# Optimization experiments

Measured on AMD Instinct MI355X. Metric: run time of the kernel, lower is better.

## Reference

```python
import jax, jax.numpy as jnp
import numpy as np

B, S, D, H = 4, 2048, 1024, 16
HS = D // H  # head size = 64


def setup_inputs() -> dict:
    key = jax.random.key(0)
    k1, k2, k3 = jax.random.split(key, 3)
    return {
        "input_data": jax.random.normal(k1, (B, S, D), dtype=jnp.float32),
        "w_qkv": jax.random.normal(k2, (D, 3 * D), dtype=jnp.float32) * (1.0 / np.sqrt(D)),
        "b_qkv": jnp.zeros((3 * D,), dtype=jnp.float32),
        "w_proj": jax.random.normal(k3, (D, D), dtype=jnp.float32) * (1.0 / np.sqrt(D)),
        "b_proj": jnp.zeros((D,), dtype=jnp.float32),
    }


def reference(input_data, w_qkv, b_qkv, w_proj, b_proj):
    b, s, d = input_data.shape
    qkv = input_data @ w_qkv + b_qkv  # [b, s, 3d]
    q, k, v = jnp.split(qkv, 3, axis=-1)
    # [b, h, s, hs]
    q = q.reshape(b, s, H, HS).transpose(0, 2, 1, 3)
    k = k.reshape(b, s, H, HS).transpose(0, 2, 1, 3)
    v = v.reshape(b, s, H, HS).transpose(0, 2, 1, 3)
    # NB: original module scales by 1/sqrt(num_heads), not 1/sqrt(head_size)
    scores = jnp.einsum('bhqd,bhkd->bhqk', q, k) / jnp.sqrt(jnp.float32(H))
    causal = jnp.tril(jnp.ones((s, s), dtype=bool))
    scores = jnp.where(causal[None, None], scores, -jnp.inf)
    weights = jax.nn.softmax(scores, axis=-1)  # dropout p=0.0 -> identity
    out = jnp.einsum('bhqk,bhkd->bhqd', weights, v)
    out = out.transpose(0, 2, 1, 3).reshape(b, s, d)
    return out @ w_proj + b_proj
```

## Files before the change

kernel.cpp:

```cpp
#include <hip/hip_runtime.h>


typedef unsigned short u16;
typedef short bf16x8 __attribute__((ext_vector_type(8)));
typedef unsigned short u16x8 __attribute__((ext_vector_type(8)));
typedef float f32x4 __attribute__((ext_vector_type(4)));
typedef float f32x16 __attribute__((ext_vector_type(16)));

#define S_LEN 2048
#define DMODEL 1024
#define NHEAD 16
#define MROWS 8192

#define SCALE_LOG2E 0.36067376022224085f

#define WAITVM_(N) asm volatile("s_waitcnt vmcnt(" #N ")" ::: "memory")
#define WAITVM(N) WAITVM_(N)

__device__ __forceinline__ u16 f2bf(float f) {
  union { float f; unsigned u; } c; c.f = f;
  unsigned u = c.u;
  u += 0x7fffu + ((u >> 16) & 1u);
  return (u16)(u >> 16);
}

__device__ __forceinline__ float exp2_fast(float x) {
  float r; asm("v_exp_f32 %0, %1" : "=v"(r) : "v"(x)); return r;
}

__device__ __forceinline__ unsigned cvtpk_bf16(float a, float b) {
  unsigned r;
  asm("v_cvt_pk_bf16_f32 %0, %1, %2" : "=v"(r) : "v"(a), "v"(b));
  return r;
}

__device__ __forceinline__ void plswap(unsigned& a, unsigned& b) {
  asm("v_permlane32_swap_b32 %0, %1" : "+v"(a), "+v"(b));
}

__device__ __forceinline__ f32x4 mfma16(bf16x8 a, bf16x8 b, f32x4 c) {
  return __builtin_amdgcn_mfma_f32_16x16x32_bf16(a, b, c, 0, 0, 0);
}

__device__ __forceinline__ f32x16 mfma32(bf16x8 a, bf16x8 b, f32x16 c) {
  return __builtin_amdgcn_mfma_f32_32x32x16_bf16(a, b, c, 0, 0, 0);
}

__device__ __forceinline__ void gload_lds16(const void* g, void* l) {
  __builtin_amdgcn_global_load_lds((__attribute__((address_space(1))) void*)g,
                                   (__attribute__((address_space(3))) void*)l,
                                   16, 0, 0);
}

__global__ void k_f32_to_bf16(const float* __restrict__ in, u16* __restrict__ out, int n) {
  int i = (blockIdx.x * 256 + threadIdx.x) * 4;
  if (i < n) {
    float4 v = *reinterpret_cast<const float4*>(in + i);
    ushort4 o;
    o.x = f2bf(v.x); o.y = f2bf(v.y); o.z = f2bf(v.z); o.w = f2bf(v.w);
    *reinterpret_cast<ushort4*>(out + i) = o;
  }
}

__global__ void k_transpose_to_bf16(const float* __restrict__ in, u16* __restrict__ out,
                                    int K, int N) {
  __shared__ float t[32][33];
  int n0 = blockIdx.x * 32, k0 = blockIdx.y * 32;
  int tx = threadIdx.x & 31, ty = threadIdx.x >> 5;
#pragma unroll
  for (int i = 0; i < 32; i += 8)
    t[ty + i][tx] = in[(size_t)(k0 + ty + i) * N + n0 + tx];
  __syncthreads();
#pragma unroll
  for (int i = 0; i < 32; i += 8)
    out[(size_t)(n0 + ty + i) * K + k0 + tx] = f2bf(t[tx][ty + i]);
}

template <int MODE>
__global__ __launch_bounds__(512, 1) void k_gemm8(const u16* __restrict__ A,
                                                  const u16* __restrict__ Bt,
                                                  const float* __restrict__ bias,
                                                  u16* __restrict__ outb,
                                                  float* __restrict__ outf,
                                                  u16* __restrict__ vtout,
                                                  int N, int K) {
  __shared__ u16 As[3][2][256 * 32];
  __shared__ u16 Bs[3][2][128 * 32];

  const int tid = threadIdx.x;
  const int lane = tid & 63, wave = tid >> 6;
  const int wr = wave >> 1, wc = wave & 1;
  const int lr = lane & 15, lk = lane >> 4;
  const int m0 = blockIdx.x * 256, n0 = blockIdx.y * 128;
  const size_t Kb = (size_t)K * 2;

  const int csw = ((tid & 3) ^ ((tid >> 3) & 3)) * 16;
  const char* Asrc0 = (const char*)A + (size_t)(m0 + (tid >> 2)) * Kb + csw;
  const char* Asrc1 = Asrc0 + 128 * Kb;
  const char* Bsrc0 = (const char*)Bt + (size_t)(n0 + (tid >> 2)) * Kb + csw;

#define STAGE_KH(BUFX, KH, T)                                                  \
  {                                                                            \
    const size_t ko_ = (size_t)(T) * 128 + (KH) * 64;                          \
    gload_lds16(Asrc0 + ko_, &As[BUFX][KH][(size_t)tid * 8]);                  \
    gload_lds16(Asrc1 + ko_, &As[BUFX][KH][((size_t)tid + 512) * 8]);          \
    gload_lds16(Bsrc0 + ko_, &Bs[BUFX][KH][(size_t)tid * 8]);                  \
  }

  f32x4 zero4 = {0.f, 0.f, 0.f, 0.f};
  f32x4 acc[4][4];
#pragma unroll
  for (int m = 0; m < 4; ++m)
#pragma unroll
    for (int n = 0; n < 4; ++n) acc[m][n] = zero4;

  const int slotsw = (lr >> 1) & 3;

#define PHASE(BUFX, KH, VM, DOSTAGE, SBUF, ST)                                 \
  {                                                                            \
    WAITVM(VM);                                                                \
    __builtin_amdgcn_s_barrier();                                              \
    __builtin_amdgcn_sched_barrier(0);                                         \
    bf16x8 af[4], bfr[4];                                                      \
    _Pragma("unroll") for (int m = 0; m < 4; ++m)                              \
        af[m] = *reinterpret_cast<const bf16x8*>(                              \
            &As[BUFX][KH][(wr * 64 + m * 16 + lr) * 32 + ((lk ^ slotsw) * 8)]);\
    _Pragma("unroll") for (int n = 0; n < 4; ++n)                              \
        bfr[n] = *reinterpret_cast<const bf16x8*>(                             \
            &Bs[BUFX][KH][(wc * 64 + n * 16 + lr) * 32 + ((lk ^ slotsw) * 8)]);\
    if (DOSTAGE) STAGE_KH(SBUF, KH, ST);                                       \
    __builtin_amdgcn_sched_barrier(0);                                         \
    __builtin_amdgcn_s_setprio(1);                                             \
    _Pragma("unroll") for (int m = 0; m < 4; ++m)                              \
        _Pragma("unroll") for (int n = 0; n < 4; ++n)                          \
            acc[m][n] = mfma16(af[m], bfr[n], acc[m][n]);                      \
    __builtin_amdgcn_s_setprio(0);                                             \
  }

  const int nkt = K >> 6;
  STAGE_KH(0, 0, 0);
  STAGE_KH(0, 1, 0);
  STAGE_KH(1, 0, 1);
  STAGE_KH(1, 1, 1);

  for (int t = 0; t < nkt - 2; ++t) {
    const int bf3 = t % 3;
    const int bn3 = (t + 2) % 3;
    PHASE(bf3, 0, 6, 1, bn3, t + 2);
    PHASE(bf3, 1, 9, 1, bn3, t + 2);
  }
  {
    const int bf3 = (nkt - 2) % 3;
    PHASE(bf3, 0, 6, 0, 0, 0);
    PHASE(bf3, 1, 6, 0, 0, 0);
  }
  {
    const int bf3 = (nkt - 1) % 3;
    PHASE(bf3, 0, 0, 0, 0, 0);
    PHASE(bf3, 1, 0, 0, 0, 0);
  }
#undef PHASE
#undef STAGE_KH

#pragma unroll
  for (int n = 0; n < 4; ++n) {
    int col = n0 + wc * 64 + n * 16 + lr;
    float bv = bias[col];
#pragma unroll
    for (int m = 0; m < 4; ++m) {
      int rowb = m0 + wr * 64 + m * 16 + lk * 4;
      if (MODE == 1) {
#pragma unroll
        for (int r = 0; r < 4; ++r)
          outf[(size_t)(rowb + r) * N + col] = acc[m][n][r] + bv;
      } else {
        if (col < 2048) {
          const float qs = (col < 1024) ? SCALE_LOG2E : 1.0f;
#pragma unroll
          for (int r = 0; r < 4; ++r)
            outb[(size_t)(rowb + r) * 2048 + col] = f2bf((acc[m][n][r] + bv) * qs);
        } else {
          int hh = (col >> 6) & 15, dd = col & 63;
          int bb = rowb >> 11, ss = rowb & 2047;
          ushort4 o;
          o.x = f2bf(acc[m][n][0] + bv);
          o.y = f2bf(acc[m][n][1] + bv);
          o.z = f2bf(acc[m][n][2] + bv);
          o.w = f2bf(acc[m][n][3] + bv);
          *reinterpret_cast<ushort4*>(
              vtout + ((size_t)(bb * 16 + hh) * 64 + dd) * 2048 + ss) = o;
        }
      }
    }
  }
}

__global__ __launch_bounds__(512, 4) void k_attn11(const u16* __restrict__ qk,
                                                   const u16* __restrict__ vt,
                                                   u16* __restrict__ ao) {
  __shared__ u16 Ks[2][4096];
  __shared__ u16 Vs[2][4096];

  const int tid = threadIdx.x;
  const int lane = tid & 63, wave = tid >> 6;
  const int l31 = lane & 31, hi = lane >> 5;
  const int gid = blockIdx.x;
  const int bh = gid & 63;
  const int tq = gid >> 6;
  const int t = (tq < 4) ? tq : 11 - tq;
  const int b = bh >> 4, h = bh & 15;

  const int q0 = t * 256 + wave * 32;
  const int ktd = (q0 + 31) >> 6;
  const int KTMAX = 4 * t + 3;
  const int qrel = q0 + l31 - ktd * 64;

  bf16x8 qf[4];
  {
    const u16* qp = qk + ((size_t)b * S_LEN + q0 + l31) * 2048 + h * 64 + hi * 8;
#pragma unroll
    for (int ks = 0; ks < 4; ++ks)
      qf[ks] = *reinterpret_cast<const bf16x8*>(qp + ks * 16);
  }

  const int swzcol = 16 * ((lane & 7) ^ (lane >> 3));
  const char* kg = (const char*)qk + ((size_t)b * S_LEN) * 4096 + 2048 + h * 128 +
                   (size_t)(wave * 8 + (lane >> 3)) * 4096 + swzcol;
  const char* vg = (const char*)vt +
                   ((size_t)bh * 64 + wave * 8 + (lane >> 3)) * 4096 + swzcol;

#define STAGE(BUF, KT)                                                   \
  {                                                                      \
    gload_lds16(kg + (size_t)(KT) * 64 * 4096, &Ks[BUF][wave * 512]);    \
    gload_lds16(vg + (size_t)(KT) * 128, &Vs[BUF][wave * 512]);          \
  }

  f32x16 oT[2];
#pragma unroll
  for (int kb = 0; kb < 2; ++kb)
#pragma unroll
    for (int e = 0; e < 16; ++e) oT[kb][e] = 0.f;
  float l_i = 0.f;

  const int rsw = (l31 & 7) << 4;

  STAGE(0, 0);
  int buf = 0;

  for (int kt = 0; kt <= KTMAX; ++kt) {
    if (kt < KTMAX) {
      STAGE(buf ^ 1, kt + 1);
      WAITVM(2);
    } else {
      WAITVM(0);
    }
    __builtin_amdgcn_s_barrier();
    __builtin_amdgcn_sched_barrier(0);

    if (kt <= ktd) {
      const char* Kb = (const char*)&Ks[buf][0];
      const char* Vb = (const char*)&Vs[buf][0];
      const bool masked = (kt == ktd);

      bf16x8 kf[2][4];
#pragma unroll
      for (int kb = 0; kb < 2; ++kb)
#pragma unroll
        for (int ks = 0; ks < 4; ++ks)
          kf[kb][ks] = *reinterpret_cast<const bf16x8*>(
              Kb + (kb * 32 + l31) * 128 + ((ks * 32 + hi * 16) ^ rsw));

      f32x16 sc[2];
      __builtin_amdgcn_s_setprio(1);
#pragma unroll
      for (int kb = 0; kb < 2; ++kb) {
        sc[kb] = mfma32(kf[kb][0], qf[0], f32x16{});
#pragma unroll
        for (int ks = 1; ks < 4; ++ks) sc[kb] = mfma32(kf[kb][ks], qf[ks], sc[kb]);
      }
      __builtin_amdgcn_s_setprio(0);

      bf16x8 vf[2][4];
#pragma unroll
      for (int kbd = 0; kbd < 2; ++kbd)
#pragma unroll
        for (int tt = 0; tt < 4; ++tt)
          vf[kbd][tt] = *reinterpret_cast<const bf16x8*>(
              Vb + (kbd * 32 + l31) * 128 + ((tt * 32 + hi * 16) ^ rsw));

      if (masked) {
#pragma unroll
        for (int kb = 0; kb < 2; ++kb)
#pragma unroll
          for (int e = 0; e < 16; ++e) {
            int key_ = kb * 32 + (e & 3) + ((e >> 2) << 3) + hi * 4;
            if (key_ > qrel) sc[kb][e] = -INFINITY;
          }
      }
      float rsa = 0.f, rsb = 0.f, rsc = 0.f, rsd = 0.f;
      unsigned pk_[8][2];
#pragma unroll
      for (int kb = 0; kb < 2; ++kb)
#pragma unroll
        for (int s = 0; s < 4; ++s) {
          float p0 = exp2_fast(sc[kb][s * 4 + 0]);
          float p1 = exp2_fast(sc[kb][s * 4 + 1]);
          float p2 = exp2_fast(sc[kb][s * 4 + 2]);
          float p3 = exp2_fast(sc[kb][s * 4 + 3]);
          rsa += p0; rsb += p1; rsc += p2; rsd += p3;
          pk_[kb * 4 + s][0] = cvtpk_bf16(p0, p1);
          pk_[kb * 4 + s][1] = cvtpk_bf16(p2, p3);
        }
      l_i += (rsa + rsb) + (rsc + rsd);

      bf16x8 pfr[4];
#pragma unroll
      for (int tt = 0; tt < 4; ++tt) {
        unsigned a0 = pk_[2 * tt][0], b0 = pk_[2 * tt + 1][0];
        unsigned a1 = pk_[2 * tt][1], b1 = pk_[2 * tt + 1][1];
        plswap(a0, b0);
        plswap(a1, b1);
        unsigned fr[4] = {a0, a1, b0, b1};
        pfr[tt] = *reinterpret_cast<const bf16x8*>(&fr[0]);
      }

      __builtin_amdgcn_s_setprio(1);
#pragma unroll
      for (int tt = 0; tt < 4; ++tt) {
        oT[0] = mfma32(vf[0][tt], pfr[tt], oT[0]);
        oT[1] = mfma32(vf[1][tt], pfr[tt], oT[1]);
      }
      __builtin_amdgcn_s_setprio(0);
    }

    __builtin_amdgcn_sched_barrier(0);
    __builtin_amdgcn_s_barrier();
    buf ^= 1;
  }
#undef STAGE

  {
    float lt = l_i + __shfl_xor(l_i, 32, 64);
    float inv = 1.f / lt;
    u16* orow = ao + ((size_t)b * S_LEN + q0 + l31) * DMODEL + h * 64 + hi * 4;
#pragma unroll
    for (int kbd = 0; kbd < 2; ++kbd)
#pragma unroll
      for (int s = 0; s < 4; ++s) {
        unsigned w0 = cvtpk_bf16(oT[kbd][s * 4 + 0] * inv, oT[kbd][s * 4 + 1] * inv);
        unsigned w1 = cvtpk_bf16(oT[kbd][s * 4 + 2] * inv, oT[kbd][s * 4 + 3] * inv);
        *reinterpret_cast<unsigned*>(orow + kbd * 32 + s * 8) = w0;
        *reinterpret_cast<unsigned*>(orow + kbd * 32 + s * 8 + 2) = w1;
      }
  }
}

extern "C" void kernel_launch(void* const* d_in, const int* in_sizes, int n_in,
                              void* d_out, int out_size, void* d_ws, size_t ws_size,
                              hipStream_t stream) {
  const float* x = (const float*)d_in[0];
  const float* wqkv = (const float*)d_in[1];
  const float* bqkv = (const float*)d_in[2];
  const float* wproj = (const float*)d_in[3];
  const float* bproj = (const float*)d_in[4];
  float* out = (float*)d_out;

  char* ws = (char*)d_ws;
  u16* Xb     = (u16*)(ws);
  u16* Wqkvt  = (u16*)(ws + (size_t)16777216);
  u16* Wprojt = (u16*)(ws + (size_t)23068672);
  u16* QKb    = (u16*)(ws + (size_t)25165824);
  u16* Vt     = (u16*)(ws + (size_t)58720256);
  u16* AOb    = (u16*)(ws + (size_t)75497472);

  k_f32_to_bf16<<<MROWS * DMODEL / 4 / 256, 256, 0, stream>>>(x, Xb, MROWS * DMODEL);
  k_transpose_to_bf16<<<dim3(3072 / 32, 1024 / 32), 256, 0, stream>>>(wqkv, Wqkvt, 1024, 3072);
  k_transpose_to_bf16<<<dim3(1024 / 32, 1024 / 32), 256, 0, stream>>>(wproj, Wprojt, 1024, 1024);

  k_gemm8<2><<<dim3(MROWS / 256, 3072 / 128), 512, 0, stream>>>(
      Xb, Wqkvt, bqkv, QKb, nullptr, Vt, 3072, 1024);

  k_attn11<<<dim3(512), 512, 0, stream>>>(QKb, Vt, AOb);

  k_gemm8<1><<<dim3(MROWS / 256, DMODEL / 128), 512, 0, stream>>>(
      AOb, Wprojt, bproj, nullptr, out, nullptr, DMODEL, 1024);
}
```

Baseline: 194.7 us.

## Restructure causal attention into small blocks pairing complementary query tiles

```diff
diff --git a/kernel.cpp b/kernel.cpp
--- a/kernel.cpp
+++ b/kernel.cpp
@@ -195,9 +195,9 @@
   }
 }
 
-__global__ __launch_bounds__(512, 4) void k_attn11(const u16* __restrict__ qk,
-                                                   const u16* __restrict__ vt,
-                                                   u16* __restrict__ ao) {
+__global__ __launch_bounds__(128) void k_attn12(const u16* __restrict__ qk,
+                                                const u16* __restrict__ vt,
+                                                u16* __restrict__ ao) {
   __shared__ u16 Ks[2][4096];
   __shared__ u16 Vs[2][4096];
 
@@ -205,90 +205,109 @@
   const int lane = tid & 63, wave = tid >> 6;
   const int l31 = lane & 31, hi = lane >> 5;
   const int gid = blockIdx.x;
-  const int bh = gid & 63;
-  const int tq = gid >> 6;
-  const int t = (tq < 4) ? tq : 11 - tq;
+  const int bh = gid >> 4, j = gid & 15;
   const int b = bh >> 4, h = bh & 15;
 
-  const int q0 = t * 256 + wave * 32;
-  const int ktd = (q0 + 31) >> 6;
-  const int KTMAX = 4 * t + 3;
-  const int qrel = q0 + l31 - ktd * 64;
-
-  bf16x8 qf[4];
+  const int A = 2 * j + wave;
+  const int Bg = 63 - A;
+  const int ktmax = 31 - j;
+  const int ktdA = j;
+  const int qrelA = ((A & 1) << 5) + l31;
+  const int qrelB = ((Bg & 1) << 5) + l31;
+  const int rowA = 32 * A, rowB = 32 * Bg;
+
+  bf16x8 qfA[4], qfB[4];
   {
-    const u16* qp = qk + ((size_t)b * S_LEN + q0 + l31) * 2048 + h * 64 + hi * 8;
-#pragma unroll
-    for (int ks = 0; ks < 4; ++ks)
-      qf[ks] = *reinterpret_cast<const bf16x8*>(qp + ks * 16);
+    const u16* qa = qk + ((size_t)b * S_LEN + rowA + l31) * 2048 + h * 64 + hi * 8;
+    const u16* qb = qk + ((size_t)b * S_LEN + rowB + l31) * 2048 + h * 64 + hi * 8;
+#pragma unroll
+    for (int ks = 0; ks < 4; ++ks) {
+      qfA[ks] = *reinterpret_cast<const bf16x8*>(qa + ks * 16);
+      qfB[ks] = *reinterpret_cast<const bf16x8*>(qb + ks * 16);
+    }
   }
 
   const int swzcol = 16 * ((lane & 7) ^ (lane >> 3));
   const char* kg = (const char*)qk + ((size_t)b * S_LEN) * 4096 + 2048 + h * 128 +
-                   (size_t)(wave * 8 + (lane >> 3)) * 4096 + swzcol;
+                   (size_t)(wave * 32 + (lane >> 3)) * 4096 + swzcol;
   const char* vg = (const char*)vt +
-                   ((size_t)bh * 64 + wave * 8 + (lane >> 3)) * 4096 + swzcol;
-
-#define STAGE(BUF, KT)                                                   \
-  {                                                                      \
-    gload_lds16(kg + (size_t)(KT) * 64 * 4096, &Ks[BUF][wave * 512]);    \
-    gload_lds16(vg + (size_t)(KT) * 128, &Vs[BUF][wave * 512]);          \
-  }
-
-  f32x16 oT[2];
-#pragma unroll
-  for (int kb = 0; kb < 2; ++kb)
-#pragma unroll
-    for (int e = 0; e < 16; ++e) oT[kb][e] = 0.f;
-  float l_i = 0.f;
+                   ((size_t)bh * 64 + wave * 32 + (lane >> 3)) * 4096 + swzcol;
+
+#define STAGE(BUF, KT)                                                        \
+  {                                                                           \
+    const char* kg_ = kg + (size_t)(KT) * 64 * 4096;                          \
+    const char* vg_ = vg + (size_t)(KT) * 128;                                \
+    _Pragma("unroll") for (int i = 0; i < 4; ++i)                             \
+        gload_lds16(kg_ + (size_t)(8 * i) * 4096,                             \
+                    &Ks[BUF][(wave * 32 + 8 * i) * 64]);                      \
+    _Pragma("unroll") for (int i = 0; i < 4; ++i)                             \
+        gload_lds16(vg_ + (size_t)(8 * i) * 4096,                             \
+                    &Vs[BUF][(wave * 32 + 8 * i) * 64]);                      \
+  }
+
+  f32x16 oT[2][2];
+#pragma unroll
+  for (int g = 0; g < 2; ++g)
+#pragma unroll
+    for (int kb = 0; kb < 2; ++kb)
+#pragma unroll
+      for (int e = 0; e < 16; ++e) oT[g][kb][e] = 0.f;
+  float l_i[2] = {0.f, 0.f};
 
   const int rsw = (l31 & 7) << 4;
 
   STAGE(0, 0);
   int buf = 0;
 
-  for (int kt = 0; kt <= KTMAX; ++kt) {
-    if (kt < KTMAX) {
+  for (int kt = 0; kt <= ktmax; ++kt) {
+    if (kt < ktmax) {
       STAGE(buf ^ 1, kt + 1);
-      WAITVM(2);
+      WAITVM(8);
     } else {
       WAITVM(0);
     }
     __builtin_amdgcn_s_barrier();
     __builtin_amdgcn_sched_barrier(0);
 
-    if (kt <= ktd) {
-      const char* Kb = (const char*)&Ks[buf][0];
-      const char* Vb = (const char*)&Vs[buf][0];
-      const bool masked = (kt == ktd);
-
-      bf16x8 kf[2][4];
-#pragma unroll
-      for (int kb = 0; kb < 2; ++kb)
-#pragma unroll
-        for (int ks = 0; ks < 4; ++ks)
-          kf[kb][ks] = *reinterpret_cast<const bf16x8*>(
-              Kb + (kb * 32 + l31) * 128 + ((ks * 32 + hi * 16) ^ rsw));
+    const char* Kb = (const char*)&Ks[buf][0];
+    const char* Vb = (const char*)&Vs[buf][0];
+
+    bf16x8 kf[2][4];
+#pragma unroll
+    for (int kb = 0; kb < 2; ++kb)
+#pragma unroll
+      for (int ks = 0; ks < 4; ++ks)
+        kf[kb][ks] = *reinterpret_cast<const bf16x8*>(
+            Kb + (kb * 32 + l31) * 128 + ((ks * 32 + hi * 16) ^ rsw));
+
+    bf16x8 vf[2][4];
+#pragma unroll
+    for (int kbd = 0; kbd < 2; ++kbd)
+#pragma unroll
+      for (int tt = 0; tt < 4; ++tt)
+        vf[kbd][tt] = *reinterpret_cast<const bf16x8*>(
+            Vb + (kbd * 32 + l31) * 128 + ((tt * 32 + hi * 16) ^ rsw));
+
+    const bool actA = (kt <= ktdA);
+
+#pragma unroll
+    for (int g = 0; g < 2; ++g) {
+      if (g == 1 && !actA) continue;
+      const bool msk = (g == 0) ? (kt == ktmax) : (kt == ktdA);
+      const int qrel = (g == 0) ? qrelB : qrelA;
 
       f32x16 sc[2];
       __builtin_amdgcn_s_setprio(1);
 #pragma unroll
       for (int kb = 0; kb < 2; ++kb) {
-        sc[kb] = mfma32(kf[kb][0], qf[0], f32x16{});
-#pragma unroll
-        for (int ks = 1; ks < 4; ++ks) sc[kb] = mfma32(kf[kb][ks], qf[ks], sc[kb]);
+        sc[kb] = mfma32(kf[kb][0], (g == 0) ? qfB[0] : qfA[0], f32x16{});
+#pragma unroll
+        for (int ks = 1; ks < 4; ++ks)
+          sc[kb] = mfma32(kf[kb][ks], (g == 0) ? qfB[ks] : qfA[ks], sc[kb]);
       }
       __builtin_amdgcn_s_setprio(0);
 
-      bf16x8 vf[2][4];
-#pragma unroll
-      for (int kbd = 0; kbd < 2; ++kbd)
-#pragma unroll
-        for (int tt = 0; tt < 4; ++tt)
-          vf[kbd][tt] = *reinterpret_cast<const bf16x8*>(
-              Vb + (kbd * 32 + l31) * 128 + ((tt * 32 + hi * 16) ^ rsw));
-
-      if (masked) {
+      if (msk) {
 #pragma unroll
         for (int kb = 0; kb < 2; ++kb)
 #pragma unroll
@@ -311,7 +330,7 @@
           pk_[kb * 4 + s][0] = cvtpk_bf16(p0, p1);
           pk_[kb * 4 + s][1] = cvtpk_bf16(p2, p3);
         }
-      l_i += (rsa + rsb) + (rsc + rsd);
+      l_i[g] += (rsa + rsb) + (rsc + rsd);
 
       bf16x8 pfr[4];
 #pragma unroll
@@ -327,8 +346,8 @@
       __builtin_amdgcn_s_setprio(1);
 #pragma unroll
       for (int tt = 0; tt < 4; ++tt) {
-        oT[0] = mfma32(vf[0][tt], pfr[tt], oT[0]);
-        oT[1] = mfma32(vf[1][tt], pfr[tt], oT[1]);
+        oT[g][0] = mfma32(vf[0][tt], pfr[tt], oT[g][0]);
+        oT[g][1] = mfma32(vf[1][tt], pfr[tt], oT[g][1]);
       }
       __builtin_amdgcn_s_setprio(0);
     }
@@ -339,16 +358,18 @@
   }
 #undef STAGE
 
-  {
-    float lt = l_i + __shfl_xor(l_i, 32, 64);
+#pragma unroll
+  for (int g = 0; g < 2; ++g) {
+    const int row0 = (g == 0) ? rowB : rowA;
+    float lt = l_i[g] + __shfl_xor(l_i[g], 32, 64);
     float inv = 1.f / lt;
-    u16* orow = ao + ((size_t)b * S_LEN + q0 + l31) * DMODEL + h * 64 + hi * 4;
+    u16* orow = ao + ((size_t)b * S_LEN + row0 + l31) * DMODEL + h * 64 + hi * 4;
 #pragma unroll
     for (int kbd = 0; kbd < 2; ++kbd)
 #pragma unroll
       for (int s = 0; s < 4; ++s) {
-        unsigned w0 = cvtpk_bf16(oT[kbd][s * 4 + 0] * inv, oT[kbd][s * 4 + 1] * inv);
-        unsigned w1 = cvtpk_bf16(oT[kbd][s * 4 + 2] * inv, oT[kbd][s * 4 + 3] * inv);
+        unsigned w0 = cvtpk_bf16(oT[g][kbd][s * 4 + 0] * inv, oT[g][kbd][s * 4 + 1] * inv);
+        unsigned w1 = cvtpk_bf16(oT[g][kbd][s * 4 + 2] * inv, oT[g][kbd][s * 4 + 3] * inv);
         *reinterpret_cast<unsigned*>(orow + kbd * 32 + s * 8) = w0;
         *reinterpret_cast<unsigned*>(orow + kbd * 32 + s * 8 + 2) = w1;
       }
@@ -380,7 +401,7 @@
   k_gemm8<2><<<dim3(MROWS / 256, 3072 / 128), 512, 0, stream>>>(
       Xb, Wqkvt, bqkv, QKb, nullptr, Vt, 3072, 1024);
 
-  k_attn11<<<dim3(512), 512, 0, stream>>>(QKb, Vt, AOb);
+  k_attn12<<<dim3(1024), 128, 0, stream>>>(QKb, Vt, AOb);
 
   k_gemm8<1><<<dim3(MROWS / 256, DMODEL / 128), 512, 0, stream>>>(
       AOb, Wprojt, bproj, nullptr, out, nullptr, DMODEL, 1024);
```

Result: no change. 196.0 us (+0.7%).
